# Performance work log

Hardware: AMD Instinct MI355X
Metric: run time of the kernel (lower is better)

The kernel has to match this reference:

```python
import jax, jax.numpy as jnp
import numpy as np

N = 4096
CIN = 128
COUT = 128
J = 2
SLOPE = 0.2        # LeakyReLU negative slope (GAT-style)
NEG = -9.0e15      # mask fill value from the source
ATT = J * COUT     # att_slice


def _leaky(v):
    return jnp.where(v >= 0, v, SLOPE * v)


def setup_inputs() -> dict:
    key = jax.random.key(0)
    ks = jax.random.split(key, 12)
    x = jax.random.normal(ks[0], (N, CIN), dtype=jnp.float32)

    def sparse_op(k):
        kv, km = jax.random.split(k)
        vals = jax.random.normal(kv, (N, N), dtype=jnp.float32)
        mask = jax.random.uniform(km, (N, N)) < 0.05
        return jnp.where(mask, vals, 0.0)

    Lu = sparse_op(ks[1])
    Ld = sparse_op(ks[2])
    P = jax.random.normal(ks[3], (N, N), dtype=jnp.float32) * 0.01  # harmonic projector

    s = 1.0 / np.sqrt(CIN)
    Wi_w = jax.random.uniform(ks[4], (J, CIN, COUT), minval=-s, maxval=s)
    Wi_b = jax.random.uniform(ks[5], (J, COUT), minval=-s, maxval=s)
    Ws_w = jax.random.uniform(ks[6], (J, CIN, COUT), minval=-s, maxval=s)
    Ws_b = jax.random.uniform(ks[7], (J, COUT), minval=-s, maxval=s)
    Wh_w = jax.random.uniform(ks[8], (CIN, COUT), minval=-s, maxval=s)
    Wh_b = jax.random.uniform(ks[9], (COUT,), minval=-s, maxval=s)
    att_irr = jax.random.normal(ks[10], (2 * ATT, 1), dtype=jnp.float32) * 0.1
    att_sol = jax.random.normal(ks[11], (2 * ATT, 1), dtype=jnp.float32) * 0.1
    return {"x": x, "Lu": Lu, "Ld": Ld, "P": P,
            "Wi_w": Wi_w, "Wi_b": Wi_b, "Ws_w": Ws_w, "Ws_b": Ws_b,
            "Wh_w": Wh_w, "Wh_b": Wh_b, "att_irr": att_irr, "att_sol": att_sol}


def reference(x, Lu, Ld, P, Wi_w, Wi_b, Ws_w, Ws_b, Wh_w, Wh_b, att_irr, att_sol):
    n = x.shape[0]
    # concat_j W_irr[j](x) -> [N, J*COUT] (j-major matches torch.cat along dim=1)
    x_irr = (jnp.einsum('nc,jco->njo', x, Wi_w) + Wi_b[None]).reshape(n, ATT)
    x_sol = (jnp.einsum('nc,jco->njo', x, Ws_w) + Ws_b[None]).reshape(n, ATT)

    # GAT-style scores: E[i,j] = leaky(s1[i] + s2[j])
    E_irr = _leaky(x_irr @ att_irr[:ATT] + (x_irr @ att_irr[ATT:]).T)
    E_sol = _leaky(x_sol @ att_sol[:ATT] + (x_sol @ att_sol[ATT:]).T)
    E_irr = jnp.where(Ld != 0, E_irr, NEG)
    E_sol = jnp.where(Lu != 0, E_sol, NEG)
    alpha_irr = jax.nn.softmax(E_irr, axis=1)  # dropout: eval mode -> identity
    alpha_sol = jax.nn.softmax(E_sol, axis=1)

    z = (alpha_irr @ x) @ Wi_w[0] + Wi_b[0] + (alpha_sol @ x) @ Ws_w[0] + Ws_b[0]
    for p in range(1, J):  # Laplacian-power aggregation
        alpha_irr = alpha_irr @ Ld
        alpha_sol = alpha_sol @ Lu
        z = z + (alpha_irr @ x) @ Wi_w[p] + Wi_b[p]
        z = z + (alpha_sol @ x) @ Ws_w[p] + Ws_b[p]
    z = z + (P @ x) @ Wh_w + Wh_b
    return z
```

## Files before the change

kernel.cpp:

```cpp
#include <hip/hip_runtime.h>

#define NN 4096
#define IDX_CAP 512
#define SLOPE 0.2f

#define V_OFF     0
#define C_OFF     512
#define BT_OFF    516
#define S_OFF     1024
#define HXI_OFF   32768
#define HXS_OFF   (HXI_OFF + NN*128)
#define UI_OFF    (HXS_OFF + NN*128)
#define US_OFF    (UI_OFF + NN*128)
#define XWH_OFF   (US_OFF + NN*128)
#define OI_OFF    (XWH_OFF + NN*128)
#define OS_OFF    (OI_OFF + NN*128)
#define ZP_OFF    (OS_OFF + NN*128)
#define WS_FLOATS (ZP_OFF + 8*NN*128)
#define IDX_BYTE_OFF ((size_t)WS_FLOATS * 4)
#define CNT_BYTE_OFF (IDX_BYTE_OFF + (size_t)2*NN*IDX_CAP*2)

__global__ __launch_bounds__(128) void k_prep(
    const float* __restrict__ Wi_w, const float* __restrict__ Wi_b,
    const float* __restrict__ Ws_w, const float* __restrict__ Ws_b,
    const float* __restrict__ Wh_b, const float* __restrict__ att_irr,
    const float* __restrict__ att_sol, float* __restrict__ ws) {
  const int t = threadIdx.x;
  float v1i = 0.f, v2i = 0.f, v1s = 0.f, v2s = 0.f;
  for (int j = 0; j < 2; ++j) {
    for (int o = 0; o < 128; ++o) {
      const float wi = Wi_w[j*16384 + t*128 + o];
      const float wv = Ws_w[j*16384 + t*128 + o];
      v1i += wi * att_irr[j*128 + o];
      v2i += wi * att_irr[256 + j*128 + o];
      v1s += wv * att_sol[j*128 + o];
      v2s += wv * att_sol[256 + j*128 + o];
    }
  }
  ws[V_OFF + t]       = v1i;
  ws[V_OFF + 128 + t] = v2i;
  ws[V_OFF + 256 + t] = v1s;
  ws[V_OFF + 384 + t] = v2s;
  ws[BT_OFF + t] = Wi_b[t] + Wi_b[128 + t] + Ws_b[t] + Ws_b[128 + t] + Wh_b[t];
  if (t < 4) {
    const float* bb = (t < 2) ? Wi_b : Ws_b;
    const float* aa = ((t < 2) ? att_irr : att_sol) + ((t & 1) ? 256 : 0);
    float c = 0.f;
    for (int k = 0; k < 256; ++k) c += bb[k] * aa[k];
    ws[C_OFF + t] = c;
  }
}

__global__ __launch_bounds__(256) void k_scores(const float* __restrict__ x,
                                                float* __restrict__ ws) {
  const int wave = threadIdx.x >> 6, lane = threadIdx.x & 63;
  const int row = blockIdx.x * 4 + wave;
  const float* v = ws + V_OFF;
  const float x0 = x[row*128 + lane];
  const float x1 = x[row*128 + 64 + lane];
  float p0 = x0 * v[lane]       + x1 * v[64 + lane];
  float p1 = x0 * v[128 + lane] + x1 * v[192 + lane];
  float p2 = x0 * v[256 + lane] + x1 * v[320 + lane];
  float p3 = x0 * v[384 + lane] + x1 * v[448 + lane];
  #pragma unroll
  for (int off = 32; off; off >>= 1) {
    p0 += __shfl_down(p0, off);
    p1 += __shfl_down(p1, off);
    p2 += __shfl_down(p2, off);
    p3 += __shfl_down(p3, off);
  }
  if (lane == 0) {
    ws[S_OFF + row]          = p0 + ws[C_OFF + 0];
    ws[S_OFF + NN + row]     = p1 + ws[C_OFF + 1];
    ws[S_OFF + 2*NN + row]   = p2 + ws[C_OFF + 2];
    ws[S_OFF + 3*NN + row]   = p3 + ws[C_OFF + 3];
  }
}

__global__ __launch_bounds__(128) void k_spmm_emit(
    const float* __restrict__ Ld, const float* __restrict__ Lu,
    const float* __restrict__ x, float* __restrict__ ws,
    unsigned short* __restrict__ idxbuf, int* __restrict__ cntbuf) {
  const int row = blockIdx.x & (NN - 1);
  const int br  = blockIdx.x >> 12;
  const float* __restrict__ Lrow = (br ? Lu : Ld) + (size_t)row * NN;
  float* __restrict__ Hx = ws + (br ? HXS_OFF : HXI_OFF);
  unsigned short* __restrict__ idx = idxbuf + (size_t)(br*NN + row) * IDX_CAP;
  const int t = threadIdx.x;

  __shared__ int   ls_cnt;
  __shared__ int   ls_j[1024];
  __shared__ float ls_v[1024];

  float acc = 0.f;
  int done = 0;
  for (int k0 = 0; k0 < NN; k0 += 1024) {
    if (t == 0) ls_cnt = 0;
    __syncthreads();
    #pragma unroll
    for (int it = 0; it < 8; ++it) {
      const int j = k0 + it*128 + t;
      const float v = Lrow[j];
      const unsigned long long m = __ballot(v != 0.f);
      const int lane = t & 63;
      int base = 0;
      if (lane == 0 && m) base = atomicAdd(&ls_cnt, (int)__popcll(m));
      base = __shfl(base, 0);
      if (v != 0.f) {
        const int pos = base + (int)__popcll(m & ((1ull << lane) - 1ull));
        ls_j[pos] = j;
        ls_v[pos] = v;
      }
    }
    __syncthreads();
    const int m = ls_cnt;
    for (int p = t; p < m; p += 128) {
      const int g = done + p;
      if (g < IDX_CAP) idx[g] = (unsigned short)ls_j[p];
    }
    int p = 0;
    for (; p + 4 <= m; p += 4) {
      const int j0 = ls_j[p], j1 = ls_j[p+1], j2 = ls_j[p+2], j3 = ls_j[p+3];
      const float v0 = ls_v[p], v1 = ls_v[p+1], v2 = ls_v[p+2], v3 = ls_v[p+3];
      const float g0 = x[j0*128 + t], g1 = x[j1*128 + t];
      const float g2 = x[j2*128 + t], g3 = x[j3*128 + t];
      acc += v0*g0; acc += v1*g1; acc += v2*g2; acc += v3*g3;
    }
    for (; p < m; ++p) acc += ls_v[p] * x[ls_j[p]*128 + t];
    done += m;
    __syncthreads();
  }
  Hx[row*128 + t] = acc;
  if (t == 0) cntbuf[br*NN + row] = done;
}

__global__ __launch_bounds__(256) void k_ugemm(
    const float* __restrict__ x, const float* __restrict__ Wi_w,
    const float* __restrict__ Ws_w, const float* __restrict__ Wh_w,
    float* __restrict__ ws) {
  const int rb = blockIdx.x;
  const int sel = blockIdx.y;
  const float* A[2]; const float* W[2]; int npass; float* out;
  if (sel == 0)      { A[0]=x; W[0]=Wi_w; A[1]=ws+HXI_OFF; W[1]=Wi_w+16384; npass=2; out=ws+UI_OFF; }
  else if (sel == 1) { A[0]=x; W[0]=Ws_w; A[1]=ws+HXS_OFF; W[1]=Ws_w+16384; npass=2; out=ws+US_OFF; }
  else               { A[0]=x; W[0]=Wh_w; A[1]=nullptr;    W[1]=nullptr;    npass=1; out=ws+XWH_OFF; }

  __shared__ __align__(16) float At[32][33];
  __shared__ __align__(16) float Wt[32][132];
  const int t = threadIdx.x;
  const int rg = t >> 4, cg = t & 15;
  const int r0 = rb * 32;
  float acc[2][8];
  #pragma unroll
  for (int i = 0; i < 2; ++i)
    #pragma unroll
    for (int j = 0; j < 8; ++j) acc[i][j] = 0.f;

  for (int ps = 0; ps < npass; ++ps) {
    const float* __restrict__ Ap = A[ps];
    const float* __restrict__ Wp = W[ps];
    for (int k0 = 0; k0 < 128; k0 += 32) {
      __syncthreads();
      {
        const int row = t >> 3, kq = t & 7;
        const float4 av = *(const float4*)&Ap[(r0 + row)*128 + k0 + kq*4];
        At[row][kq*4+0] = av.x; At[row][kq*4+1] = av.y;
        At[row][kq*4+2] = av.z; At[row][kq*4+3] = av.w;
      }
      #pragma unroll
      for (int l = 0; l < 4; ++l) {
        const int idx = t + l*256;
        const int kr = idx >> 5, c4 = idx & 31;
        const float4 wv = *(const float4*)&Wp[(k0 + kr)*128 + c4*4];
        Wt[kr][c4*4+0] = wv.x; Wt[kr][c4*4+1] = wv.y;
        Wt[kr][c4*4+2] = wv.z; Wt[kr][c4*4+3] = wv.w;
      }
      __syncthreads();
      #pragma unroll
      for (int k = 0; k < 32; ++k) {
        const float a0 = At[rg*2 + 0][k];
        const float a1 = At[rg*2 + 1][k];
        const float4 b0 = *(const float4*)&Wt[k][cg*8];
        const float4 b1 = *(const float4*)&Wt[k][cg*8 + 4];
        acc[0][0] += a0*b0.x; acc[0][1] += a0*b0.y; acc[0][2] += a0*b0.z; acc[0][3] += a0*b0.w;
        acc[0][4] += a0*b1.x; acc[0][5] += a0*b1.y; acc[0][6] += a0*b1.z; acc[0][7] += a0*b1.w;
        acc[1][0] += a1*b0.x; acc[1][1] += a1*b0.y; acc[1][2] += a1*b0.z; acc[1][3] += a1*b0.w;
        acc[1][4] += a1*b1.x; acc[1][5] += a1*b1.y; acc[1][6] += a1*b1.z; acc[1][7] += a1*b1.w;
      }
    }
  }
  #pragma unroll
  for (int i = 0; i < 2; ++i) {
    const int r = r0 + rg*2 + i;
    #pragma unroll
    for (int j = 0; j < 8; ++j) out[r*128 + cg*8 + j] = acc[i][j];
  }
}

__global__ __launch_bounds__(256) void k_pgemm(const float* __restrict__ P,
                                               const float* __restrict__ ws,
                                               float* __restrict__ zpart) {
  const int rbl = blockIdx.x;
  const int kz  = blockIdx.y;
  const float* __restrict__ Xw = ws + XWH_OFF;

  __shared__ __align__(16) float Pt[64][33];
  __shared__ __align__(16) float Xt[32][132];
  const int t = threadIdx.x;
  const int rg = t >> 4, cg = t & 15;
  const int r0 = rbl * 64;
  const int kbase = kz * 512;
  float acc[4][8];
  #pragma unroll
  for (int i = 0; i < 4; ++i)
    #pragma unroll
    for (int j = 0; j < 8; ++j) acc[i][j] = 0.f;

  for (int k0 = kbase; k0 < kbase + 512; k0 += 32) {
    __syncthreads();
    #pragma unroll
    for (int l = 0; l < 2; ++l) {
      const int idx = t + l*256;
      const int row = idx >> 3, kq = idx & 7;
      const float4 pv = *(const float4*)&P[(size_t)(r0 + row)*NN + k0 + kq*4];
      Pt[row][kq*4+0] = pv.x; Pt[row][kq*4+1] = pv.y;
      Pt[row][kq*4+2] = pv.z; Pt[row][kq*4+3] = pv.w;
    }
    #pragma unroll
    for (int l = 0; l < 4; ++l) {
      const int idx = t + l*256;
      const int kr = idx >> 5, c4 = idx & 31;
      const float4 xv = *(const float4*)&Xw[(k0 + kr)*128 + c4*4];
      Xt[kr][c4*4+0] = xv.x; Xt[kr][c4*4+1] = xv.y;
      Xt[kr][c4*4+2] = xv.z; Xt[kr][c4*4+3] = xv.w;
    }
    __syncthreads();
    #pragma unroll
    for (int k = 0; k < 32; ++k) {
      const float a0 = Pt[rg*4 + 0][k];
      const float a1 = Pt[rg*4 + 1][k];
      const float a2 = Pt[rg*4 + 2][k];
      const float a3 = Pt[rg*4 + 3][k];
      const float4 b0 = *(const float4*)&Xt[k][cg*8];
      const float4 b1 = *(const float4*)&Xt[k][cg*8 + 4];
      acc[0][0] += a0*b0.x; acc[0][1] += a0*b0.y; acc[0][2] += a0*b0.z; acc[0][3] += a0*b0.w;
      acc[0][4] += a0*b1.x; acc[0][5] += a0*b1.y; acc[0][6] += a0*b1.z; acc[0][7] += a0*b1.w;
      acc[1][0] += a1*b0.x; acc[1][1] += a1*b0.y; acc[1][2] += a1*b0.z; acc[1][3] += a1*b0.w;
      acc[1][4] += a1*b1.x; acc[1][5] += a1*b1.y; acc[1][6] += a1*b1.z; acc[1][7] += a1*b1.w;
      acc[2][0] += a2*b0.x; acc[2][1] += a2*b0.y; acc[2][2] += a2*b0.z; acc[2][3] += a2*b0.w;
      acc[2][4] += a2*b1.x; acc[2][5] += a2*b1.y; acc[2][6] += a2*b1.z; acc[2][7] += a2*b1.w;
      acc[3][0] += a3*b0.x; acc[3][1] += a3*b0.y; acc[3][2] += a3*b0.z; acc[3][3] += a3*b0.w;
      acc[3][4] += a3*b1.x; acc[3][5] += a3*b1.y; acc[3][6] += a3*b1.z; acc[3][7] += a3*b1.w;
    }
  }
  float* __restrict__ zp = zpart + (size_t)kz * NN * 128;
  #pragma unroll
  for (int i = 0; i < 4; ++i) {
    const int r = r0 + rg*4 + i;
    #pragma unroll
    for (int j = 0; j < 8; ++j) zp[r*128 + cg*8 + j] = acc[i][j];
  }
}

__global__ __launch_bounds__(256) void k_attn(
    const float* __restrict__ Ld, const float* __restrict__ Lu,
    float* __restrict__ ws, const unsigned short* __restrict__ idxbuf,
    const int* __restrict__ cntbuf) {
  const int row = blockIdx.x & (NN - 1);
  const int br  = blockIdx.x >> 12;
  const float* __restrict__ U = ws + (br ? US_OFF : UI_OFF);
  float* __restrict__ O = ws + (br ? OS_OFF : OI_OFF);
  const float s1 = ws[S_OFF + (br ? 2*NN : 0) + row];
  const float* __restrict__ s2a = ws + S_OFF + (br ? 3*NN : NN);
  const int cnt = cntbuf[br*NN + row];
  const int t = threadIdx.x;
  const int col = t & 127;
  const int half = t >> 7;

  __shared__ int   jl[IDX_CAP];
  __shared__ float el[IDX_CAP];
  __shared__ float red[256];
  __shared__ float dsh[2];

  float acc = 0.f;
  if (cnt > 0 && cnt <= IDX_CAP) {
    const unsigned short* __restrict__ idx = idxbuf + (size_t)(br*NN + row) * IDX_CAP;
    float dpart = 0.f;
    for (int p = t; p < cnt; p += 256) {
      const int j = idx[p];
      const float sc = s1 + s2a[j];
      const float e = expf(sc >= 0.f ? sc : SLOPE * sc);
      jl[p] = j; el[p] = e; dpart += e;
    }
    red[t] = dpart;
    __syncthreads();
    if (t < 128) red[t] += red[t + 128];
    __syncthreads();
    if (t < 64) {
      float v = red[t] + red[t + 64];
      #pragma unroll
      for (int off = 32; off; off >>= 1) v += __shfl_down(v, off);
      if (t == 0) dsh[0] = v;
    }
    __syncthreads();
    const float den = dsh[0];
    int p = half;
    for (; p + 8 <= cnt; p += 8) {
      const int j0 = jl[p], j1 = jl[p+2], j2 = jl[p+4], j3 = jl[p+6];
      const float e0 = el[p], e1 = el[p+2], e2 = el[p+4], e3 = el[p+6];
      const float g0 = U[j0*128 + col], g1 = U[j1*128 + col];
      const float g2 = U[j2*128 + col], g3 = U[j3*128 + col];
      acc += e0*g0; acc += e1*g1; acc += e2*g2; acc += e3*g3;
    }
    for (; p < cnt; p += 2) acc += el[p] * U[jl[p]*128 + col];
    red[t] = acc;
    __syncthreads();
    if (t < 128) O[row*128 + t] = (red[t] + red[t + 128]) / den;
  } else if (cnt == 0) {
    for (int j = half; j < NN; j += 2) acc += U[j*128 + col];
    red[t] = acc;
    __syncthreads();
    if (t < 128) O[row*128 + t] = (red[t] + red[t + 128]) * (1.f / NN);
  } else {
    const float* __restrict__ Lrow = (br ? Lu : Ld) + (size_t)row * NN;
    float dpart = 0.f;
    for (int j = half; j < NN; j += 2) {
      const float v = Lrow[j];
      if (v != 0.f) {
        const float sc = s1 + s2a[j];
        const float e = expf(sc >= 0.f ? sc : SLOPE * sc);
        if (col == 0) dpart += e;
        acc += e * U[j*128 + col];
      }
    }
    if (col == 0) dsh[half] = dpart;
    red[t] = acc;
    __syncthreads();
    const float den = dsh[0] + dsh[1];
    if (t < 128) O[row*128 + t] = (red[t] + red[t + 128]) / den;
  }
}

__global__ __launch_bounds__(256) void k_combine(const float* __restrict__ ws,
                                                 float* __restrict__ z) {
  const int i = blockIdx.x * 256 + threadIdx.x;
  const int col = i & 127;
  float acc = ws[BT_OFF + col] + ws[OI_OFF + i] + ws[OS_OFF + i];
  #pragma unroll
  for (int kz = 0; kz < 8; ++kz) acc += ws[ZP_OFF + kz*NN*128 + i];
  z[i] = acc;
}

extern "C" void kernel_launch(void* const* d_in, const int* in_sizes, int n_in,
                              void* d_out, int out_size, void* d_ws, size_t ws_size,
                              hipStream_t stream) {
  const float* x       = (const float*)d_in[0];
  const float* Lu      = (const float*)d_in[1];
  const float* Ld      = (const float*)d_in[2];
  const float* P       = (const float*)d_in[3];
  const float* Wi_w    = (const float*)d_in[4];
  const float* Wi_b    = (const float*)d_in[5];
  const float* Ws_w    = (const float*)d_in[6];
  const float* Ws_b    = (const float*)d_in[7];
  const float* Wh_w    = (const float*)d_in[8];
  const float* Wh_b    = (const float*)d_in[9];
  const float* att_irr = (const float*)d_in[10];
  const float* att_sol = (const float*)d_in[11];
  float* z  = (float*)d_out;
  float* ws = (float*)d_ws;
  unsigned short* idxbuf = (unsigned short*)((char*)d_ws + IDX_BYTE_OFF);
  int*            cntbuf = (int*)((char*)d_ws + CNT_BYTE_OFF);

  k_prep<<<1, 128, 0, stream>>>(Wi_w, Wi_b, Ws_w, Ws_b, Wh_b, att_irr, att_sol, ws);
  k_scores<<<1024, 256, 0, stream>>>(x, ws);
  k_spmm_emit<<<2 * NN, 128, 0, stream>>>(Ld, Lu, x, ws, idxbuf, cntbuf);
  {
    dim3 g(128, 3);
    k_ugemm<<<g, 256, 0, stream>>>(x, Wi_w, Ws_w, Wh_w, ws);
  }
  {
    dim3 g(64, 8);
    k_pgemm<<<g, 256, 0, stream>>>(P, ws, ws + ZP_OFF);
  }
  k_attn<<<2 * NN, 256, 0, stream>>>(Ld, Lu, ws, idxbuf, cntbuf);
  k_combine<<<NN * 128 / 256, 256, 0, stream>>>(ws, z);
}
```

Measured before the change: 434.2 us.

## Restructure sparse gather kernels with float4 row scan and wave-split float2 gathers

The sparse row kernel now uses 256 threads. It loads each dense Laplacian row with float4 loads in a single pass instead of four 1024-column chunks with barriers. The gather-accumulate over nonzeros is split across four waves, each lane handling two columns via float2 loads, with a shared-memory reduction across waves. The attention kernel's gather is restructured the same way. The aim is more memory-level parallelism and fewer barriers in these bandwidth-bound kernels, at the cost of extra shared memory and a cross-wave reduction.

```diff
diff --git a/kernel.cpp b/kernel.cpp
--- a/kernel.cpp
+++ b/kernel.cpp
@@ -77,7 +77,7 @@
   }
 }
 
-__global__ __launch_bounds__(128) void k_spmm_emit(
+__global__ __launch_bounds__(256) void k_spmm_emit(
     const float* __restrict__ Ld, const float* __restrict__ Lu,
     const float* __restrict__ x, float* __restrict__ ws,
     unsigned short* __restrict__ idxbuf, int* __restrict__ cntbuf) {
@@ -85,53 +85,78 @@
   const int br  = blockIdx.x >> 12;
   const float* __restrict__ Lrow = (br ? Lu : Ld) + (size_t)row * NN;
   float* __restrict__ Hx = ws + (br ? HXS_OFF : HXI_OFF);
-  unsigned short* __restrict__ idx = idxbuf + (size_t)(br*NN + row) * IDX_CAP;
+  unsigned short* __restrict__ idxg = idxbuf + (size_t)(br*NN + row) * IDX_CAP;
+  const float2* __restrict__ x2 = (const float2*)x;
   const int t = threadIdx.x;
-
-  __shared__ int   ls_cnt;
-  __shared__ int   ls_j[1024];
-  __shared__ float ls_v[1024];
-
-  float acc = 0.f;
-  int done = 0;
-  for (int k0 = 0; k0 < NN; k0 += 1024) {
-    if (t == 0) ls_cnt = 0;
-    __syncthreads();
-    #pragma unroll
-    for (int it = 0; it < 8; ++it) {
-      const int j = k0 + it*128 + t;
-      const float v = Lrow[j];
+  const int w = t >> 6, lane = t & 63;
+
+  __shared__ int   cnt;
+  __shared__ int   jl[IDX_CAP];
+  __shared__ float vl[IDX_CAP];
+  __shared__ float red[4][128];
+
+  if (t == 0) cnt = 0;
+  __syncthreads();
+
+  const float4* __restrict__ Lrow4 = (const float4*)Lrow;
+  float4 lv[4];
+  #pragma unroll
+  for (int i = 0; i < 4; ++i) lv[i] = Lrow4[i*256 + t];
+  #pragma unroll
+  for (int i = 0; i < 4; ++i) {
+    #pragma unroll
+    for (int c = 0; c < 4; ++c) {
+      const float v = (&lv[i].x)[c];
       const unsigned long long m = __ballot(v != 0.f);
-      const int lane = t & 63;
       int base = 0;
-      if (lane == 0 && m) base = atomicAdd(&ls_cnt, (int)__popcll(m));
+      if (lane == 0 && m) base = atomicAdd(&cnt, (int)__popcll(m));
       base = __shfl(base, 0);
       if (v != 0.f) {
         const int pos = base + (int)__popcll(m & ((1ull << lane) - 1ull));
-        ls_j[pos] = j;
-        ls_v[pos] = v;
-      }
-    }
-    __syncthreads();
-    const int m = ls_cnt;
-    for (int p = t; p < m; p += 128) {
-      const int g = done + p;
-      if (g < IDX_CAP) idx[g] = (unsigned short)ls_j[p];
-    }
-    int p = 0;
-    for (; p + 4 <= m; p += 4) {
-      const int j0 = ls_j[p], j1 = ls_j[p+1], j2 = ls_j[p+2], j3 = ls_j[p+3];
-      const float v0 = ls_v[p], v1 = ls_v[p+1], v2 = ls_v[p+2], v3 = ls_v[p+3];
-      const float g0 = x[j0*128 + t], g1 = x[j1*128 + t];
-      const float g2 = x[j2*128 + t], g3 = x[j3*128 + t];
-      acc += v0*g0; acc += v1*g1; acc += v2*g2; acc += v3*g3;
-    }
-    for (; p < m; ++p) acc += ls_v[p] * x[ls_j[p]*128 + t];
-    done += m;
-    __syncthreads();
-  }
-  Hx[row*128 + t] = acc;
-  if (t == 0) cntbuf[br*NN + row] = done;
+        if (pos < IDX_CAP) { jl[pos] = (i*256 + t)*4 + c; vl[pos] = v; }
+      }
+    }
+  }
+  __syncthreads();
+  const int m = cnt;
+
+  for (int p = t; p < m && p < IDX_CAP; p += 256) idxg[p] = (unsigned short)jl[p];
+  if (t == 0) cntbuf[br*NN + row] = m;
+
+  float acc0 = 0.f, acc1 = 0.f;
+  if (m <= IDX_CAP) {
+    int p = w;
+    for (; p + 12 < m; p += 16) {
+      const int j0 = jl[p], j1 = jl[p+4], j2 = jl[p+8], j3 = jl[p+12];
+      const float v0 = vl[p], v1 = vl[p+4], v2 = vl[p+8], v3 = vl[p+12];
+      const float2 g0 = x2[j0*64 + lane];
+      const float2 g1 = x2[j1*64 + lane];
+      const float2 g2 = x2[j2*64 + lane];
+      const float2 g3 = x2[j3*64 + lane];
+      acc0 += v0*g0.x; acc1 += v0*g0.y;
+      acc0 += v1*g1.x; acc1 += v1*g1.y;
+      acc0 += v2*g2.x; acc1 += v2*g2.y;
+      acc0 += v3*g3.x; acc1 += v3*g3.y;
+    }
+    for (; p < m; p += 4) {
+      const int j = jl[p]; const float v = vl[p];
+      const float2 g = x2[j*64 + lane];
+      acc0 += v*g.x; acc1 += v*g.y;
+    }
+  } else {
+    for (int j = w*1024; j < (w+1)*1024; ++j) {
+      const float v = Lrow[j];
+      if (v != 0.f) {
+        const float2 g = x2[j*64 + lane];
+        acc0 += v*g.x; acc1 += v*g.y;
+      }
+    }
+  }
+  red[w][lane*2]     = acc0;
+  red[w][lane*2 + 1] = acc1;
+  __syncthreads();
+  if (t < 128)
+    Hx[row*128 + t] = red[0][t] + red[1][t] + red[2][t] + red[3][t];
 }
 
 __global__ __launch_bounds__(256) void k_ugemm(
@@ -269,20 +294,21 @@
   const int row = blockIdx.x & (NN - 1);
   const int br  = blockIdx.x >> 12;
   const float* __restrict__ U = ws + (br ? US_OFF : UI_OFF);
+  const float2* __restrict__ U2 = (const float2*)U;
   float* __restrict__ O = ws + (br ? OS_OFF : OI_OFF);
   const float s1 = ws[S_OFF + (br ? 2*NN : 0) + row];
   const float* __restrict__ s2a = ws + S_OFF + (br ? 3*NN : NN);
   const int cnt = cntbuf[br*NN + row];
   const int t = threadIdx.x;
-  const int col = t & 127;
-  const int half = t >> 7;
+  const int w = t >> 6, lane = t & 63;
 
   __shared__ int   jl[IDX_CAP];
   __shared__ float el[IDX_CAP];
-  __shared__ float red[256];
-  __shared__ float dsh[2];
-
-  float acc = 0.f;
+  __shared__ float red[4][128];
+  __shared__ float rsum[256];
+  __shared__ float dsh[4];
+
+  float acc0 = 0.f, acc1 = 0.f;
   if (cnt > 0 && cnt <= IDX_CAP) {
     const unsigned short* __restrict__ idx = idxbuf + (size_t)(br*NN + row) * IDX_CAP;
     float dpart = 0.f;
@@ -292,52 +318,71 @@
       const float e = expf(sc >= 0.f ? sc : SLOPE * sc);
       jl[p] = j; el[p] = e; dpart += e;
     }
-    red[t] = dpart;
-    __syncthreads();
-    if (t < 128) red[t] += red[t + 128];
+    rsum[t] = dpart;
+    __syncthreads();
+    if (t < 128) rsum[t] += rsum[t + 128];
     __syncthreads();
     if (t < 64) {
-      float v = red[t] + red[t + 64];
+      float v = rsum[t] + rsum[t + 64];
       #pragma unroll
       for (int off = 32; off; off >>= 1) v += __shfl_down(v, off);
       if (t == 0) dsh[0] = v;
     }
     __syncthreads();
     const float den = dsh[0];
-    int p = half;
-    for (; p + 8 <= cnt; p += 8) {
-      const int j0 = jl[p], j1 = jl[p+2], j2 = jl[p+4], j3 = jl[p+6];
-      const float e0 = el[p], e1 = el[p+2], e2 = el[p+4], e3 = el[p+6];
-      const float g0 = U[j0*128 + col], g1 = U[j1*128 + col];
-      const float g2 = U[j2*128 + col], g3 = U[j3*128 + col];
-      acc += e0*g0; acc += e1*g1; acc += e2*g2; acc += e3*g3;
-    }
-    for (; p < cnt; p += 2) acc += el[p] * U[jl[p]*128 + col];
-    red[t] = acc;
-    __syncthreads();
-    if (t < 128) O[row*128 + t] = (red[t] + red[t + 128]) / den;
+    int p = w;
+    for (; p + 12 < cnt; p += 16) {
+      const int j0 = jl[p], j1 = jl[p+4], j2 = jl[p+8], j3 = jl[p+12];
+      const float e0 = el[p], e1 = el[p+4], e2 = el[p+8], e3 = el[p+12];
+      const float2 g0 = U2[j0*64 + lane];
+      const float2 g1 = U2[j1*64 + lane];
+      const float2 g2 = U2[j2*64 + lane];
+      const float2 g3 = U2[j3*64 + lane];
+      acc0 += e0*g0.x; acc1 += e0*g0.y;
+      acc0 += e1*g1.x; acc1 += e1*g1.y;
+      acc0 += e2*g2.x; acc1 += e2*g2.y;
+      acc0 += e3*g3.x; acc1 += e3*g3.y;
+    }
+    for (; p < cnt; p += 4) {
+      const int j = jl[p]; const float e = el[p];
+      const float2 g = U2[j*64 + lane];
+      acc0 += e*g.x; acc1 += e*g.y;
+    }
+    red[w][lane*2]     = acc0;
+    red[w][lane*2 + 1] = acc1;
+    __syncthreads();
+    if (t < 128)
+      O[row*128 + t] = (red[0][t] + red[1][t] + red[2][t] + red[3][t]) / den;
   } else if (cnt == 0) {
-    for (int j = half; j < NN; j += 2) acc += U[j*128 + col];
-    red[t] = acc;
-    __syncthreads();
-    if (t < 128) O[row*128 + t] = (red[t] + red[t + 128]) * (1.f / NN);
+    for (int j = w*1024; j < (w+1)*1024; ++j) {
+      const float2 g = U2[j*64 + lane];
+      acc0 += g.x; acc1 += g.y;
+    }
+    red[w][lane*2]     = acc0;
+    red[w][lane*2 + 1] = acc1;
+    __syncthreads();
+    if (t < 128)
+      O[row*128 + t] = (red[0][t] + red[1][t] + red[2][t] + red[3][t]) * (1.f / NN);
   } else {
     const float* __restrict__ Lrow = (br ? Lu : Ld) + (size_t)row * NN;
-    float dpart = 0.f;
-    for (int j = half; j < NN; j += 2) {
+    float dp = 0.f;
+    for (int j = w*1024; j < (w+1)*1024; ++j) {
       const float v = Lrow[j];
       if (v != 0.f) {
         const float sc = s1 + s2a[j];
         const float e = expf(sc >= 0.f ? sc : SLOPE * sc);
-        if (col == 0) dpart += e;
-        acc += e * U[j*128 + col];
-      }
-    }
-    if (col == 0) dsh[half] = dpart;
-    red[t] = acc;
-    __syncthreads();
-    const float den = dsh[0] + dsh[1];
-    if (t < 128) O[row*128 + t] = (red[t] + red[t + 128]) / den;
+        const float2 g = U2[j*64 + lane];
+        acc0 += e*g.x; acc1 += e*g.y;
+        dp += e;
+      }
+    }
+    if (lane == 0) dsh[w] = dp;
+    red[w][lane*2]     = acc0;
+    red[w][lane*2 + 1] = acc1;
+    __syncthreads();
+    const float den = dsh[0] + dsh[1] + dsh[2] + dsh[3];
+    if (t < 128)
+      O[row*128 + t] = (red[0][t] + red[1][t] + red[2][t] + red[3][t]) / den;
   }
 }
 
@@ -373,7 +418,7 @@
 
   k_prep<<<1, 128, 0, stream>>>(Wi_w, Wi_b, Ws_w, Ws_b, Wh_b, att_irr, att_sol, ws);
   k_scores<<<1024, 256, 0, stream>>>(x, ws);
-  k_spmm_emit<<<2 * NN, 128, 0, stream>>>(Ld, Lu, x, ws, idxbuf, cntbuf);
+  k_spmm_emit<<<2 * NN, 256, 0, stream>>>(Ld, Lu, x, ws, idxbuf, cntbuf);
   {
     dim3 g(128, 3);
     k_ugemm<<<g, 256, 0, stream>>>(x, Wi_w, Ws_w, Wh_w, ws);
```

Measured after the change: 400.0 us. 1.09x faster.

## Split dense-to-CSR compaction from SpMM and use wave-per-row gathers

Applied to the files above, without the earlier changes.

Replaces the fused scan+SpMM kernel with a separate CSR build: an atomic-count kernel with four waves per row that stores both indices and values, then a wave-per-row gather kernel that broadcasts indices via shuffles and reads float2 rows of x. The attention kernel is likewise rewritten to one wave per row with shuffle-based reduction and no shared memory or block barriers. The P GEMM stores its A tile transposed for float4 LDS reads. This adds an extra launch and a value buffer, and the CSR order within a row becomes nondeterministic under atomics.

```diff
diff --git a/kernel.cpp b/kernel.cpp
--- a/kernel.cpp
+++ b/kernel.cpp
@@ -1,7 +1,7 @@
 #include <hip/hip_runtime.h>
 
 #define NN 4096
-#define IDX_CAP 512
+#define CAP 384
 #define SLOPE 0.2f
 
 #define V_OFF     0
@@ -18,7 +18,8 @@
 #define ZP_OFF    (OS_OFF + NN*128)
 #define WS_FLOATS (ZP_OFF + 8*NN*128)
 #define IDX_BYTE_OFF ((size_t)WS_FLOATS * 4)
-#define CNT_BYTE_OFF (IDX_BYTE_OFF + (size_t)2*NN*IDX_CAP*2)
+#define VAL_BYTE_OFF (IDX_BYTE_OFF + (size_t)2*NN*CAP*2)
+#define CNT_BYTE_OFF (VAL_BYTE_OFF + (size_t)2*NN*CAP*4)
 
 __global__ __launch_bounds__(128) void k_prep(
     const float* __restrict__ Wi_w, const float* __restrict__ Wi_b,
@@ -77,61 +78,115 @@
   }
 }
 
-__global__ __launch_bounds__(128) void k_spmm_emit(
+__global__ __launch_bounds__(256) void k_zero(int* __restrict__ cnt) {
+  cnt[blockIdx.x * 256 + threadIdx.x] = 0;
+}
+
+__global__ __launch_bounds__(256) void k_csr(
+    const float* __restrict__ Ld, const float* __restrict__ Lu,
+    int* __restrict__ cntbuf, unsigned short* __restrict__ idxb,
+    float* __restrict__ valb) {
+  const int w = threadIdx.x >> 6, lane = threadIdx.x & 63;
+  const int W = blockIdx.x * 4 + w;
+  const int br = W >> 14;
+  const int row = (W >> 2) & (NN - 1);
+  const int quarter = W & 3;
+  const float4* __restrict__ L4 =
+      (const float4*)((br ? Lu : Ld) + (size_t)row * NN + quarter * 1024);
+  float4 lv[4];
+  #pragma unroll
+  for (int i = 0; i < 4; ++i) lv[i] = L4[i*64 + lane];
+
+  unsigned long long m[16];
+  int runs[16];
+  int run = 0;
+  #pragma unroll
+  for (int i = 0; i < 4; ++i)
+    #pragma unroll
+    for (int c = 0; c < 4; ++c) {
+      const int r = i*4 + c;
+      m[r] = __ballot((&lv[i].x)[c] != 0.f);
+      runs[r] = run;
+      run += (int)__popcll(m[r]);
+    }
+  int base = 0;
+  if (lane == 0 && run) base = atomicAdd(&cntbuf[br*NN + row], run);
+  base = __shfl(base, 0);
+  const size_t rb = (size_t)(br*NN + row) * CAP;
+  const unsigned long long lmask = (1ull << lane) - 1ull;
+  #pragma unroll
+  for (int i = 0; i < 4; ++i)
+    #pragma unroll
+    for (int c = 0; c < 4; ++c) {
+      const int r = i*4 + c;
+      const float v = (&lv[i].x)[c];
+      if (v != 0.f) {
+        const int pos = base + runs[r] + (int)__popcll(m[r] & lmask);
+        if (pos < CAP) {
+          idxb[rb + pos] = (unsigned short)(quarter*1024 + (i*64 + lane)*4 + c);
+          valb[rb + pos] = v;
+        }
+      }
+    }
+}
+
+__global__ __launch_bounds__(256) void k_gather_hx(
     const float* __restrict__ Ld, const float* __restrict__ Lu,
     const float* __restrict__ x, float* __restrict__ ws,
-    unsigned short* __restrict__ idxbuf, int* __restrict__ cntbuf) {
-  const int row = blockIdx.x & (NN - 1);
-  const int br  = blockIdx.x >> 12;
-  const float* __restrict__ Lrow = (br ? Lu : Ld) + (size_t)row * NN;
-  float* __restrict__ Hx = ws + (br ? HXS_OFF : HXI_OFF);
-  unsigned short* __restrict__ idx = idxbuf + (size_t)(br*NN + row) * IDX_CAP;
-  const int t = threadIdx.x;
-
-  __shared__ int   ls_cnt;
-  __shared__ int   ls_j[1024];
-  __shared__ float ls_v[1024];
-
-  float acc = 0.f;
-  int done = 0;
-  for (int k0 = 0; k0 < NN; k0 += 1024) {
-    if (t == 0) ls_cnt = 0;
-    __syncthreads();
-    #pragma unroll
-    for (int it = 0; it < 8; ++it) {
-      const int j = k0 + it*128 + t;
+    const unsigned short* __restrict__ idxb, const float* __restrict__ valb,
+    const int* __restrict__ cntbuf) {
+  const int w = threadIdx.x >> 6, lane = threadIdx.x & 63;
+  const int W = blockIdx.x * 4 + w;
+  const int br = W >> 12;
+  const int row = W & (NN - 1);
+  const float2* __restrict__ x2 = (const float2*)x;
+  float2* __restrict__ Hx2 = (float2*)(ws + (br ? HXS_OFF : HXI_OFF));
+  const int cnt = cntbuf[br*NN + row];
+  float a0 = 0.f, a1 = 0.f;
+  if (cnt <= CAP) {
+    const size_t rb = (size_t)(br*NN + row) * CAP;
+    int jv[6]; float vv[6];
+    #pragma unroll
+    for (int s = 0; s < 6; ++s) {
+      const int p = s*64 + lane;
+      const bool in = p < cnt;
+      jv[s] = in ? (int)idxb[rb + p] : 0;
+      vv[s] = in ? valb[rb + p] : 0.f;
+    }
+    #pragma unroll
+    for (int s = 0; s < 6; ++s) {
+      if (s*64 < cnt) {
+        const int qn = min(64, cnt - s*64);
+        const int jvs = jv[s]; const float vvs = vv[s];
+        int q = 0;
+        for (; q + 8 <= qn; q += 8) {
+          const int j0=__shfl(jvs,q+0), j1=__shfl(jvs,q+1), j2=__shfl(jvs,q+2), j3=__shfl(jvs,q+3);
+          const int j4=__shfl(jvs,q+4), j5=__shfl(jvs,q+5), j6=__shfl(jvs,q+6), j7=__shfl(jvs,q+7);
+          const float v0=__shfl(vvs,q+0), v1=__shfl(vvs,q+1), v2=__shfl(vvs,q+2), v3=__shfl(vvs,q+3);
+          const float v4=__shfl(vvs,q+4), v5=__shfl(vvs,q+5), v6=__shfl(vvs,q+6), v7=__shfl(vvs,q+7);
+          const float2 g0=x2[j0*64+lane], g1=x2[j1*64+lane], g2=x2[j2*64+lane], g3=x2[j3*64+lane];
+          const float2 g4=x2[j4*64+lane], g5=x2[j5*64+lane], g6=x2[j6*64+lane], g7=x2[j7*64+lane];
+          a0+=v0*g0.x; a1+=v0*g0.y; a0+=v1*g1.x; a1+=v1*g1.y;
+          a0+=v2*g2.x; a1+=v2*g2.y; a0+=v3*g3.x; a1+=v3*g3.y;
+          a0+=v4*g4.x; a1+=v4*g4.y; a0+=v5*g5.x; a1+=v5*g5.y;
+          a0+=v6*g6.x; a1+=v6*g6.y; a0+=v7*g7.x; a1+=v7*g7.y;
+        }
+        for (; q < qn; ++q) {
+          const int j = __shfl(jvs, q); const float v = __shfl(vvs, q);
+          const float2 g = x2[j*64+lane];
+          a0 += v*g.x; a1 += v*g.y;
+        }
+      }
+    }
+  } else {
+    const float* __restrict__ Lrow = (br ? Lu : Ld) + (size_t)row * NN;
+    for (int j = 0; j < NN; ++j) {
       const float v = Lrow[j];
-      const unsigned long long m = __ballot(v != 0.f);
-      const int lane = t & 63;
-      int base = 0;
-      if (lane == 0 && m) base = atomicAdd(&ls_cnt, (int)__popcll(m));
-      base = __shfl(base, 0);
-      if (v != 0.f) {
-        const int pos = base + (int)__popcll(m & ((1ull << lane) - 1ull));
-        ls_j[pos] = j;
-        ls_v[pos] = v;
-      }
-    }
-    __syncthreads();
-    const int m = ls_cnt;
-    for (int p = t; p < m; p += 128) {
-      const int g = done + p;
-      if (g < IDX_CAP) idx[g] = (unsigned short)ls_j[p];
-    }
-    int p = 0;
-    for (; p + 4 <= m; p += 4) {
-      const int j0 = ls_j[p], j1 = ls_j[p+1], j2 = ls_j[p+2], j3 = ls_j[p+3];
-      const float v0 = ls_v[p], v1 = ls_v[p+1], v2 = ls_v[p+2], v3 = ls_v[p+3];
-      const float g0 = x[j0*128 + t], g1 = x[j1*128 + t];
-      const float g2 = x[j2*128 + t], g3 = x[j3*128 + t];
-      acc += v0*g0; acc += v1*g1; acc += v2*g2; acc += v3*g3;
-    }
-    for (; p < m; ++p) acc += ls_v[p] * x[ls_j[p]*128 + t];
-    done += m;
-    __syncthreads();
-  }
-  Hx[row*128 + t] = acc;
-  if (t == 0) cntbuf[br*NN + row] = done;
+      if (v != 0.f) { const float2 g = x2[j*64+lane]; a0 += v*g.x; a1 += v*g.y; }
+    }
+  }
+  float2 o; o.x = a0; o.y = a1;
+  Hx2[row*64 + lane] = o;
 }
 
 __global__ __launch_bounds__(256) void k_ugemm(
@@ -161,12 +216,10 @@
     const float* __restrict__ Wp = W[ps];
     for (int k0 = 0; k0 < 128; k0 += 32) {
       __syncthreads();
-      {
-        const int row = t >> 3, kq = t & 7;
+      { const int row = t >> 3, kq = t & 7;
         const float4 av = *(const float4*)&Ap[(r0 + row)*128 + k0 + kq*4];
         At[row][kq*4+0] = av.x; At[row][kq*4+1] = av.y;
-        At[row][kq*4+2] = av.z; At[row][kq*4+3] = av.w;
-      }
+        At[row][kq*4+2] = av.z; At[row][kq*4+3] = av.w; }
       #pragma unroll
       for (int l = 0; l < 4; ++l) {
         const int idx = t + l*256;
@@ -204,7 +257,7 @@
   const int kz  = blockIdx.y;
   const float* __restrict__ Xw = ws + XWH_OFF;
 
-  __shared__ __align__(16) float Pt[64][33];
+  __shared__ __align__(16) float At[32][68];
   __shared__ __align__(16) float Xt[32][132];
   const int t = threadIdx.x;
   const int rg = t >> 4, cg = t & 15;
@@ -223,8 +276,8 @@
       const int idx = t + l*256;
       const int row = idx >> 3, kq = idx & 7;
       const float4 pv = *(const float4*)&P[(size_t)(r0 + row)*NN + k0 + kq*4];
-      Pt[row][kq*4+0] = pv.x; Pt[row][kq*4+1] = pv.y;
-      Pt[row][kq*4+2] = pv.z; Pt[row][kq*4+3] = pv.w;
+      At[kq*4+0][row] = pv.x; At[kq*4+1][row] = pv.y;
+      At[kq*4+2][row] = pv.z; At[kq*4+3][row] = pv.w;
     }
     #pragma unroll
     for (int l = 0; l < 4; ++l) {
@@ -237,20 +290,17 @@
     __syncthreads();
     #pragma unroll
     for (int k = 0; k < 32; ++k) {
-      const float a0 = Pt[rg*4 + 0][k];
-      const float a1 = Pt[rg*4 + 1][k];
-      const float a2 = Pt[rg*4 + 2][k];
-      const float a3 = Pt[rg*4 + 3][k];
+      const float4 a  = *(const float4*)&At[k][rg*4];
       const float4 b0 = *(const float4*)&Xt[k][cg*8];
       const float4 b1 = *(const float4*)&Xt[k][cg*8 + 4];
-      acc[0][0] += a0*b0.x; acc[0][1] += a0*b0.y; acc[0][2] += a0*b0.z; acc[0][3] += a0*b0.w;
-      acc[0][4] += a0*b1.x; acc[0][5] += a0*b1.y; acc[0][6] += a0*b1.z; acc[0][7] += a0*b1.w;
-      acc[1][0] += a1*b0.x; acc[1][1] += a1*b0.y; acc[1][2] += a1*b0.z; acc[1][3] += a1*b0.w;
-      acc[1][4] += a1*b1.x; acc[1][5] += a1*b1.y; acc[1][6] += a1*b1.z; acc[1][7] += a1*b1.w;
-      acc[2][0] += a2*b0.x; acc[2][1] += a2*b0.y; acc[2][2] += a2*b0.z; acc[2][3] += a2*b0.w;
-      acc[2][4] += a2*b1.x; acc[2][5] += a2*b1.y; acc[2][6] += a2*b1.z; acc[2][7] += a2*b1.w;
-      acc[3][0] += a3*b0.x; acc[3][1] += a3*b0.y; acc[3][2] += a3*b0.z; acc[3][3] += a3*b0.w;
-      acc[3][4] += a3*b1.x; acc[3][5] += a3*b1.y; acc[3][6] += a3*b1.z; acc[3][7] += a3*b1.w;
+      acc[0][0] += a.x*b0.x; acc[0][1] += a.x*b0.y; acc[0][2] += a.x*b0.z; acc[0][3] += a.x*b0.w;
+      acc[0][4] += a.x*b1.x; acc[0][5] += a.x*b1.y; acc[0][6] += a.x*b1.z; acc[0][7] += a.x*b1.w;
+      acc[1][0] += a.y*b0.x; acc[1][1] += a.y*b0.y; acc[1][2] += a.y*b0.z; acc[1][3] += a.y*b0.w;
+      acc[1][4] += a.y*b1.x; acc[1][5] += a.y*b1.y; acc[1][6] += a.y*b1.z; acc[1][7] += a.y*b1.w;
+      acc[2][0] += a.z*b0.x; acc[2][1] += a.z*b0.y; acc[2][2] += a.z*b0.z; acc[2][3] += a.z*b0.w;
+      acc[2][4] += a.z*b1.x; acc[2][5] += a.z*b1.y; acc[2][6] += a.z*b1.z; acc[2][7] += a.z*b1.w;
+      acc[3][0] += a.w*b0.x; acc[3][1] += a.w*b0.y; acc[3][2] += a.w*b0.z; acc[3][3] += a.w*b0.w;
+      acc[3][4] += a.w*b1.x; acc[3][5] += a.w*b1.y; acc[3][6] += a.w*b1.z; acc[3][7] += a.w*b1.w;
     }
   }
   float* __restrict__ zp = zpart + (size_t)kz * NN * 128;
@@ -264,80 +314,81 @@
 
 __global__ __launch_bounds__(256) void k_attn(
     const float* __restrict__ Ld, const float* __restrict__ Lu,
-    float* __restrict__ ws, const unsigned short* __restrict__ idxbuf,
+    float* __restrict__ ws, const unsigned short* __restrict__ idxb,
     const int* __restrict__ cntbuf) {
-  const int row = blockIdx.x & (NN - 1);
-  const int br  = blockIdx.x >> 12;
-  const float* __restrict__ U = ws + (br ? US_OFF : UI_OFF);
-  float* __restrict__ O = ws + (br ? OS_OFF : OI_OFF);
+  const int w = threadIdx.x >> 6, lane = threadIdx.x & 63;
+  const int W = blockIdx.x * 4 + w;
+  const int br = W >> 12;
+  const int row = W & (NN - 1);
+  const float2* __restrict__ U2 = (const float2*)(ws + (br ? US_OFF : UI_OFF));
+  float2* __restrict__ O2 = (float2*)(ws + (br ? OS_OFF : OI_OFF));
   const float s1 = ws[S_OFF + (br ? 2*NN : 0) + row];
   const float* __restrict__ s2a = ws + S_OFF + (br ? 3*NN : NN);
   const int cnt = cntbuf[br*NN + row];
-  const int t = threadIdx.x;
-  const int col = t & 127;
-  const int half = t >> 7;
-
-  __shared__ int   jl[IDX_CAP];
-  __shared__ float el[IDX_CAP];
-  __shared__ float red[256];
-  __shared__ float dsh[2];
-
-  float acc = 0.f;
-  if (cnt > 0 && cnt <= IDX_CAP) {
-    const unsigned short* __restrict__ idx = idxbuf + (size_t)(br*NN + row) * IDX_CAP;
-    float dpart = 0.f;
-    for (int p = t; p < cnt; p += 256) {
-      const int j = idx[p];
-      const float sc = s1 + s2a[j];
-      const float e = expf(sc >= 0.f ? sc : SLOPE * sc);
-      jl[p] = j; el[p] = e; dpart += e;
-    }
-    red[t] = dpart;
-    __syncthreads();
-    if (t < 128) red[t] += red[t + 128];
-    __syncthreads();
-    if (t < 64) {
-      float v = red[t] + red[t + 64];
-      #pragma unroll
-      for (int off = 32; off; off >>= 1) v += __shfl_down(v, off);
-      if (t == 0) dsh[0] = v;
-    }
-    __syncthreads();
-    const float den = dsh[0];
-    int p = half;
-    for (; p + 8 <= cnt; p += 8) {
-      const int j0 = jl[p], j1 = jl[p+2], j2 = jl[p+4], j3 = jl[p+6];
-      const float e0 = el[p], e1 = el[p+2], e2 = el[p+4], e3 = el[p+6];
-      const float g0 = U[j0*128 + col], g1 = U[j1*128 + col];
-      const float g2 = U[j2*128 + col], g3 = U[j3*128 + col];
-      acc += e0*g0; acc += e1*g1; acc += e2*g2; acc += e3*g3;
-    }
-    for (; p < cnt; p += 2) acc += el[p] * U[jl[p]*128 + col];
-    red[t] = acc;
-    __syncthreads();
-    if (t < 128) O[row*128 + t] = (red[t] + red[t + 128]) / den;
+  float a0 = 0.f, a1 = 0.f;
+  float den = 0.f;
+
+  if (cnt > 0 && cnt <= CAP) {
+    const size_t rb = (size_t)(br*NN + row) * CAP;
+    int jv[6]; float ev[6];
+    float dl = 0.f;
+    #pragma unroll
+    for (int s = 0; s < 6; ++s) {
+      const int p = s*64 + lane;
+      if (p < cnt) {
+        const int j = (int)idxb[rb + p];
+        const float sc = s1 + s2a[j];
+        const float e = expf(sc >= 0.f ? sc : SLOPE * sc);
+        jv[s] = j; ev[s] = e; dl += e;
+      } else { jv[s] = 0; ev[s] = 0.f; }
+    }
+    #pragma unroll
+    for (int off = 32; off; off >>= 1) dl += __shfl_xor(dl, off);
+    den = dl;
+    #pragma unroll
+    for (int s = 0; s < 6; ++s) {
+      if (s*64 < cnt) {
+        const int qn = min(64, cnt - s*64);
+        const int jvs = jv[s]; const float evs = ev[s];
+        int q = 0;
+        for (; q + 8 <= qn; q += 8) {
+          const int j0=__shfl(jvs,q+0), j1=__shfl(jvs,q+1), j2=__shfl(jvs,q+2), j3=__shfl(jvs,q+3);
+          const int j4=__shfl(jvs,q+4), j5=__shfl(jvs,q+5), j6=__shfl(jvs,q+6), j7=__shfl(jvs,q+7);
+          const float e0=__shfl(evs,q+0), e1=__shfl(evs,q+1), e2=__shfl(evs,q+2), e3=__shfl(evs,q+3);
+          const float e4=__shfl(evs,q+4), e5=__shfl(evs,q+5), e6=__shfl(evs,q+6), e7=__shfl(evs,q+7);
+          const float2 g0=U2[j0*64+lane], g1=U2[j1*64+lane], g2=U2[j2*64+lane], g3=U2[j3*64+lane];
+          const float2 g4=U2[j4*64+lane], g5=U2[j5*64+lane], g6=U2[j6*64+lane], g7=U2[j7*64+lane];
+          a0+=e0*g0.x; a1+=e0*g0.y; a0+=e1*g1.x; a1+=e1*g1.y;
+          a0+=e2*g2.x; a1+=e2*g2.y; a0+=e3*g3.x; a1+=e3*g3.y;
+          a0+=e4*g4.x; a1+=e4*g4.y; a0+=e5*g5.x; a1+=e5*g5.y;
+          a0+=e6*g6.x; a1+=e6*g6.y; a0+=e7*g7.x; a1+=e7*g7.y;
+        }
+        for (; q < qn; ++q) {
+          const int j = __shfl(jvs, q); const float e = __shfl(evs, q);
+          const float2 g = U2[j*64+lane];
+          a0 += e*g.x; a1 += e*g.y;
+        }
+      }
+    }
+    float2 o; o.x = a0 / den; o.y = a1 / den;
+    O2[row*64 + lane] = o;
   } else if (cnt == 0) {
-    for (int j = half; j < NN; j += 2) acc += U[j*128 + col];
-    red[t] = acc;
-    __syncthreads();
-    if (t < 128) O[row*128 + t] = (red[t] + red[t + 128]) * (1.f / NN);
+    for (int j = 0; j < NN; ++j) { const float2 g = U2[j*64+lane]; a0 += g.x; a1 += g.y; }
+    float2 o; o.x = a0 * (1.f/NN); o.y = a1 * (1.f/NN);
+    O2[row*64 + lane] = o;
   } else {
     const float* __restrict__ Lrow = (br ? Lu : Ld) + (size_t)row * NN;
-    float dpart = 0.f;
-    for (int j = half; j < NN; j += 2) {
+    for (int j = 0; j < NN; ++j) {
       const float v = Lrow[j];
       if (v != 0.f) {
         const float sc = s1 + s2a[j];
         const float e = expf(sc >= 0.f ? sc : SLOPE * sc);
-        if (col == 0) dpart += e;
-        acc += e * U[j*128 + col];
-      }
-    }
-    if (col == 0) dsh[half] = dpart;
-    red[t] = acc;
-    __syncthreads();
-    const float den = dsh[0] + dsh[1];
-    if (t < 128) O[row*128 + t] = (red[t] + red[t + 128]) / den;
+        const float2 g = U2[j*64+lane];
+        a0 += e*g.x; a1 += e*g.y; den += e;
+      }
+    }
+    float2 o; o.x = a0 / den; o.y = a1 / den;
+    O2[row*64 + lane] = o;
   }
 }
 
@@ -368,12 +419,15 @@
   const float* att_sol = (const float*)d_in[11];
   float* z  = (float*)d_out;
   float* ws = (float*)d_ws;
-  unsigned short* idxbuf = (unsigned short*)((char*)d_ws + IDX_BYTE_OFF);
-  int*            cntbuf = (int*)((char*)d_ws + CNT_BYTE_OFF);
+  unsigned short* idxb = (unsigned short*)((char*)d_ws + IDX_BYTE_OFF);
+  float*          valb = (float*)((char*)d_ws + VAL_BYTE_OFF);
+  int*            cntb = (int*)((char*)d_ws + CNT_BYTE_OFF);
 
   k_prep<<<1, 128, 0, stream>>>(Wi_w, Wi_b, Ws_w, Ws_b, Wh_b, att_irr, att_sol, ws);
   k_scores<<<1024, 256, 0, stream>>>(x, ws);
-  k_spmm_emit<<<2 * NN, 128, 0, stream>>>(Ld, Lu, x, ws, idxbuf, cntbuf);
+  k_zero<<<32, 256, 0, stream>>>(cntb);
+  k_csr<<<8192, 256, 0, stream>>>(Ld, Lu, cntb, idxb, valb);
+  k_gather_hx<<<2048, 256, 0, stream>>>(Ld, Lu, x, ws, idxb, valb, cntb);
   {
     dim3 g(128, 3);
     k_ugemm<<<g, 256, 0, stream>>>(x, Wi_w, Ws_w, Wh_w, ws);
@@ -382,6 +436,6 @@
     dim3 g(64, 8);
     k_pgemm<<<g, 256, 0, stream>>>(P, ws, ws + ZP_OFF);
   }
-  k_attn<<<2 * NN, 256, 0, stream>>>(Ld, Lu, ws, idxbuf, cntbuf);
+  k_attn<<<2048, 256, 0, stream>>>(Ld, Lu, ws, idxb, cntb);
   k_combine<<<NN * 128 / 256, 256, 0, stream>>>(ws, z);
 }
```

Result: faster. 415.7 us (-4.3%).
